# Kernel optimization log

Hardware: AMD Instinct MI355X
Metric: run time of the kernel (lower is better)

## Reference

```python
import jax, jax.numpy as jnp
import numpy as np

T, D, N, H = 2032, 1408, 16, 88  # K == N (MHA vision attention)
BLOCK_SIZE = 128
ROPE_THETA = 10000.0


def _apply_rope_interleaved(x_tnh, freqs_cis):
    # x_tnh: [T, N, H]; freqs_cis: [T, H//2, 2] with (..., 0)=cos, (..., 1)=sin.
    cos = freqs_cis[:, None, :, 0]  # [T, 1, H//2]
    sin = freqs_cis[:, None, :, 1]
    x1 = x_tnh[..., 0::2]
    x2 = x_tnh[..., 1::2]
    # interleaved rotation: pairs (even, odd) rotated by angle theta_t
    rot = jnp.stack([x1 * cos - x2 * sin, x1 * sin + x2 * cos], axis=-1)
    return rot.reshape(x_tnh.shape)


def setup_inputs() -> dict:
    key = jax.random.key(0)
    ks = jax.random.split(key, 10)
    s = 0.02
    x = jax.random.normal(ks[0], (T, D), dtype=jnp.float32)
    # precomputed rotary cos/sin table (interleaved ordering)
    pos = jnp.arange(T, dtype=jnp.float32)
    inv_freq = ROPE_THETA ** (-jnp.arange(0, H, 2, dtype=jnp.float32) / H)  # [H//2]
    ang = pos[:, None] * inv_freq[None, :]                                  # [T, H//2]
    freqs_cis = jnp.stack([jnp.cos(ang), jnp.sin(ang)], axis=-1)            # [T, H//2, 2]
    Wq = jax.random.normal(ks[1], (D, N, H), dtype=jnp.float32) * s
    Wk = jax.random.normal(ks[2], (D, N, H), dtype=jnp.float32) * s
    Wv = jax.random.normal(ks[3], (D, N, H), dtype=jnp.float32) * s
    Wo = jax.random.normal(ks[4], (N, H, D), dtype=jnp.float32) * s
    bq = jax.random.normal(ks[5], (N, H), dtype=jnp.float32) * s
    bk = jax.random.normal(ks[6], (N, H), dtype=jnp.float32) * s
    bv = jax.random.normal(ks[7], (N, H), dtype=jnp.float32) * s
    bo = jax.random.normal(ks[8], (D,), dtype=jnp.float32) * s
    return {"x": x, "freqs_cis": freqs_cis, "Wq": Wq, "bq": bq, "Wk": Wk,
            "bk": bk, "Wv": Wv, "bv": bv, "Wo": Wo, "bo": bo}


def reference(x, freqs_cis, Wq, bq, Wk, bk, Wv, bv, Wo, bo):
    t, d = x.shape
    n, h = bq.shape
    sm_scale = h ** -0.5
    # fused QKV projections + bias + RoPE (q, k only)
    q = jnp.einsum('td,dnh->tnh', x, Wq) + bq[None]
    q = _apply_rope_interleaved(q, freqs_cis)
    k = jnp.einsum('td,dkh->tkh', x, Wk) + bk[None]
    k = _apply_rope_interleaved(k, freqs_cis)
    v = jnp.einsum('td,dkh->tkh', x, Wv) + bv[None]
    # pad T up to a multiple of BLOCK_SIZE, as the flash-attention call requires
    pad_len = (BLOCK_SIZE - t % BLOCK_SIZE) % BLOCK_SIZE
    qp = jnp.pad(q, ((0, pad_len), (0, 0), (0, 0)))
    kp = jnp.pad(k, ((0, pad_len), (0, 0), (0, 0)))
    vp = jnp.pad(v, ((0, pad_len), (0, 0), (0, 0)))
    # [N, Tp, H]
    qh = jnp.transpose(qp, (1, 0, 2))
    kh = jnp.transpose(kp, (1, 0, 2))
    vh = jnp.transpose(vp, (1, 0, 2))
    # segment ids: 0 for valid tokens, 1 for padding; attention only within equal ids
    seg = jnp.concatenate([jnp.zeros((t,), jnp.int32), jnp.ones((pad_len,), jnp.int32)])
    mask = seg[:, None] == seg[None, :]  # [Tp, Tp]
    scores = jnp.einsum('nth,nsh->nts', qh, kh) * sm_scale
    scores = jnp.where(mask[None], scores, jnp.finfo(scores.dtype).min)
    probs = jax.nn.softmax(scores, axis=-1)
    out = jnp.einsum('nts,nsh->nth', probs, vh)        # [N, Tp, H]
    out = jnp.transpose(out, (1, 0, 2))[:t]            # [T, N, H]
    o = jnp.einsum('tnh,nhd->td', out, Wo) + bo
    return o
```

## Files before the change

kernel.cpp:

```cpp
#include <hip/hip_runtime.h>
#include <hip/hip_bf16.h>
#include <stdint.h>
#include <stddef.h>

typedef __bf16 bf16_t;
typedef __bf16 bf16x8 __attribute__((ext_vector_type(8)));
typedef __bf16 bf16x4 __attribute__((ext_vector_type(4)));
typedef float  f32x4  __attribute__((ext_vector_type(4)));

#define T_SEQ 2032
#define T_PAD 2048
#define DM    1408
#define NHEAD 16
#define HD    88
#define HP    96
#define KVB   128
#define NT    (T_PAD / KVB)
#define SM_SCALE 0.10660035817780521f
#define LOG2E 1.4426950408889634f
#define DEFER_THR 8.0f

__device__ __forceinline__ void gload_lds16(const bf16_t* g, bf16_t* l) {
  __builtin_amdgcn_global_load_lds(
      (__attribute__((address_space(1))) void*)(g),
      (__attribute__((address_space(3))) void*)(l), 16, 0, 0);
}

__global__ void k_convert_x(const float* __restrict__ x, bf16_t* __restrict__ Xb) {
  int idx = blockIdx.x * 256 + threadIdx.x;
  const int total = T_PAD * DM / 4;
  if (idx >= total) return;
  int base = idx * 4;
  int t = base / DM;
  float4 v;
  if (t < T_SEQ) v = *(const float4*)(x + base);
  else           v = make_float4(0.f, 0.f, 0.f, 0.f);
  bf16x4 o;
  o[0] = (bf16_t)v.x; o[1] = (bf16_t)v.y; o[2] = (bf16_t)v.z; o[3] = (bf16_t)v.w;
  *(bf16x4*)(Xb + base) = o;
}

__global__ void k_transpose4(const float* __restrict__ W0, const float* __restrict__ W1,
                             const float* __restrict__ W2, const float* __restrict__ W3,
                             bf16_t* __restrict__ d012, bf16_t* __restrict__ d3) {
  const int which = blockIdx.x / 484;
  const int b = blockIdx.x % 484;
  const float* src = (which == 0) ? W0 : (which == 1) ? W1 : (which == 2) ? W2 : W3;
  bf16_t* dst = (which < 3) ? (d012 + (size_t)which * DM * DM) : d3;
  const int tr = b / 22, tc = b % 22;
  __shared__ float tile[64][65];
  const int t = threadIdx.x;
  const int row = t >> 2, l4 = t & 3;
#pragma unroll
  for (int i = 0; i < 4; ++i) {
    float4 v = *(const float4*)(src + (size_t)(tr * 64 + row) * DM + tc * 64 + l4 * 16 + i * 4);
    *(float4*)&tile[row][l4 * 16 + i * 4] = v;
  }
  __syncthreads();
  const int jj = t >> 2;
#pragma unroll
  for (int it = 0; it < 2; ++it) {
    const int c = (t & 3) + 4 * it;
    bf16x8 o;
#pragma unroll
    for (int e = 0; e < 8; ++e) o[e] = (bf16_t)tile[c * 8 + e][jj];
    *(bf16x8*)(dst + (size_t)(tc * 64 + jj) * DM + tr * 64 + c * 8) = o;
  }
}

__device__ __forceinline__ void gemm_main_1408(
    const bf16_t* __restrict__ A, const bf16_t* __restrict__ Bt,
    bf16_t* As, bf16_t* Bs,
    int m0, int n0, f32x4 acc[4][4]) {
  const int tid = threadIdx.x;
  const int w = tid >> 6, lane = tid & 63;
  const int l15 = lane & 15, lg = lane >> 4;
  const int b0 = w * 2048 + lane * 16;
  const int r0 = b0 >> 6, k0 = (b0 & 63) >> 1;
  const int b1 = b0 + 1024;
  const int r1 = b1 >> 6, k1 = (b1 & 63) >> 1;
  const int wr = w >> 1, wc = w & 1;
  const size_t aoff0 = (size_t)(m0 + r0) * DM + k0;
  const size_t aoff1 = (size_t)(m0 + r1) * DM + k1;
  const size_t boff0 = (size_t)(n0 + r0) * DM + k0;
  const size_t boff1 = (size_t)(n0 + r1) * DM + k1;
  gload_lds16(A + aoff0, As + w * 1024);
  gload_lds16(A + aoff1, As + w * 1024 + 512);
  gload_lds16(Bt + boff0, Bs + w * 1024);
  gload_lds16(Bt + boff1, Bs + w * 1024 + 512);
  for (int kt = 0; kt < 44; ++kt) {
    const int cur = kt & 1;
    const int kon = ((kt < 43) ? kt + 1 : 43) * 32;
    const int db = (cur ^ 1) * 4096;
    gload_lds16(A + aoff0 + kon, As + db + w * 1024);
    gload_lds16(A + aoff1 + kon, As + db + w * 1024 + 512);
    gload_lds16(Bt + boff0 + kon, Bs + db + w * 1024);
    gload_lds16(Bt + boff1 + kon, Bs + db + w * 1024 + 512);
    asm volatile("s_waitcnt vmcnt(4)" ::: "memory");
    __builtin_amdgcn_s_barrier();
    const bf16_t* Ac = As + cur * 4096;
    const bf16_t* Bc = Bs + cur * 4096;
    bf16x8 av[4], bv[4];
#pragma unroll
    for (int m = 0; m < 4; ++m)
      av[m] = *(const bf16x8*)(Ac + (wr * 64 + m * 16 + l15) * 32 + lg * 8);
#pragma unroll
    for (int n = 0; n < 4; ++n)
      bv[n] = *(const bf16x8*)(Bc + (wc * 64 + n * 16 + l15) * 32 + lg * 8);
    __builtin_amdgcn_s_setprio(1);
#pragma unroll
    for (int m = 0; m < 4; ++m)
#pragma unroll
      for (int n = 0; n < 4; ++n)
        acc[m][n] = __builtin_amdgcn_mfma_f32_16x16x32_bf16(av[m], bv[n], acc[m][n], 0, 0, 0);
    __builtin_amdgcn_s_setprio(0);
    __builtin_amdgcn_s_barrier();
  }
  asm volatile("s_waitcnt vmcnt(0)" ::: "memory");
}

__global__ __launch_bounds__(256, 2) void k_gemm_qkv(
    const bf16_t* __restrict__ A, const bf16_t* __restrict__ Bt,
    const float* __restrict__ bq, const float* __restrict__ bk,
    const float* __restrict__ bvp, const float* __restrict__ freqs,
    bf16_t* __restrict__ Qh, bf16_t* __restrict__ Kh, bf16_t* __restrict__ Vt) {
  __shared__ bf16_t As[2 * 4096];
  __shared__ bf16_t Bs[2 * 4096];
  const int bid = blockIdx.x;
  const int sbid = (bid & 7) * 66 + (bid >> 3);
  const int mt = sbid / 33, nt = sbid % 33;
  f32x4 acc[4][4];
#pragma unroll
  for (int m = 0; m < 4; ++m)
#pragma unroll
    for (int n = 0; n < 4; ++n) acc[m][n] = (f32x4){0.f, 0.f, 0.f, 0.f};
  gemm_main_1408(A, Bt, As, Bs, mt * 128, nt * 128, acc);
  const int tid = threadIdx.x, w = tid >> 6, lane = tid & 63;
  const int l15 = lane & 15, lg = lane >> 4;
  const int wr = w >> 1, wc = w & 1;
  const int cb = nt * 128 + wc * 64, rb = mt * 128 + wr * 64;
#pragma unroll
  for (int n = 0; n < 4; ++n) {
    const int col = cb + n * 16 + l15;
    const int seg = (col >= 2 * DM) ? 2 : ((col >= DM) ? 1 : 0);
    const int cc = col - seg * DM;
    const float* bp = (seg == 0) ? bq : (seg == 1) ? bk : bvp;
    const float bval = bp[cc];
    const int hn = cc / 88;
    const int hh = cc - hn * 88;
    const int hbase = hh & ~1;
    const bool odd = hh & 1;
#pragma unroll
    for (int m = 0; m < 4; ++m) {
      const int tb = rb + m * 16 + lg * 4;
      if (seg == 2) {
        bf16x4 vv;
#pragma unroll
        for (int r = 0; r < 4; ++r) vv[r] = (bf16_t)(acc[m][n][r] + bval);
        *(bf16x4*)(Vt + ((size_t)hn * HP + hh) * T_PAD + tb) = vv;
      } else {
#pragma unroll
        for (int r = 0; r < 4; ++r) {
          const int t = tb + r;
          const float v = acc[m][n][r] + bval;
          const float p = __shfl_xor(v, 1);
          const int tc2 = (t < T_SEQ) ? t : 0;
          const float c = freqs[tc2 * 88 + hbase];
          const float s = freqs[tc2 * 88 + hbase + 1];
          const float x1 = odd ? p : v;
          const float x2 = odd ? v : p;
          const float ro = odd ? (x1 * s + x2 * c) : (x1 * c - x2 * s);
          if (seg == 0)
            Qh[((size_t)hn * T_PAD + t) * HP + hh] = (bf16_t)(ro * (SM_SCALE * LOG2E));
          else
            Kh[((size_t)hn * T_PAD + t) * HP + hh] = (bf16_t)ro;
        }
      }
    }
  }
}

__global__ __launch_bounds__(256, 2) void k_gemm_out64(
    const bf16_t* __restrict__ A, const bf16_t* __restrict__ Bt,
    const float* __restrict__ bo, float* __restrict__ out) {
  __shared__ bf16_t Sm[2 * 6144];
  const int bid = blockIdx.x;
  const int sbid = (bid & 7) * 44 + (bid >> 3);
  const int mt = sbid / 11, nt = sbid % 11;
  const int m0 = mt * 64, n0 = nt * 128;
  const int tid = threadIdx.x, w = tid >> 6, lane = tid & 63;
  const int l15 = lane & 15, lg = lane >> 4;
  const bf16_t* srcp[3];
  size_t srco[3];
  int dste[3];
#pragma unroll
  for (int p = 0; p < 3; ++p) {
    const int off = w * 3072 + p * 1024;
    const int o = off + lane * 16;
    dste[p] = off >> 1;
    if (off < 4096) {
      int r = o >> 6, k = (o & 63) >> 1;
      srcp[p] = A; srco[p] = (size_t)(m0 + r) * DM + k;
    } else {
      int ob = o - 4096;
      int r = ob >> 6, k = (ob & 63) >> 1;
      srcp[p] = Bt; srco[p] = (size_t)(n0 + r) * DM + k;
    }
  }
  f32x4 acc[4][2];
#pragma unroll
  for (int m = 0; m < 4; ++m)
#pragma unroll
    for (int n = 0; n < 2; ++n) acc[m][n] = (f32x4){0.f, 0.f, 0.f, 0.f};
#pragma unroll
  for (int p = 0; p < 3; ++p) gload_lds16(srcp[p] + srco[p], Sm + dste[p]);
  for (int kt = 0; kt < 44; ++kt) {
    const int cur = kt & 1;
    const int kon = ((kt < 43) ? kt + 1 : 43) * 32;
    const int db = (cur ^ 1) * 6144;
#pragma unroll
    for (int p = 0; p < 3; ++p)
      gload_lds16(srcp[p] + srco[p] + kon, Sm + db + dste[p]);
    asm volatile("s_waitcnt vmcnt(3)" ::: "memory");
    __builtin_amdgcn_s_barrier();
    const bf16_t* Sc = Sm + cur * 6144;
    bf16x8 av[4], bv2[2];
#pragma unroll
    for (int m = 0; m < 4; ++m)
      av[m] = *(const bf16x8*)(Sc + (m * 16 + l15) * 32 + lg * 8);
#pragma unroll
    for (int n = 0; n < 2; ++n)
      bv2[n] = *(const bf16x8*)(Sc + 2048 + (w * 32 + n * 16 + l15) * 32 + lg * 8);
    __builtin_amdgcn_s_setprio(1);
#pragma unroll
    for (int m = 0; m < 4; ++m)
#pragma unroll
      for (int n = 0; n < 2; ++n)
        acc[m][n] = __builtin_amdgcn_mfma_f32_16x16x32_bf16(av[m], bv2[n], acc[m][n], 0, 0, 0);
    __builtin_amdgcn_s_setprio(0);
    __builtin_amdgcn_s_barrier();
  }
  asm volatile("s_waitcnt vmcnt(0)" ::: "memory");
  const int cb = n0 + w * 32;
#pragma unroll
  for (int n = 0; n < 2; ++n) {
    const int col = cb + n * 16 + l15;
    const float bval = bo[col];
#pragma unroll
    for (int m = 0; m < 4; ++m) {
#pragma unroll
      for (int r = 0; r < 4; ++r) {
        const int t = m0 + m * 16 + lg * 4 + r;
        if (t < T_SEQ) out[(size_t)t * DM + col] = acc[m][n][r] + bval;
      }
    }
  }
}

__global__ __launch_bounds__(256, 2) void k_attn(
    const bf16_t* __restrict__ Qh, const bf16_t* __restrict__ Kh,
    const bf16_t* __restrict__ Vt, bf16_t* __restrict__ Ob) {
  __shared__ bf16_t Ps[4][16 * 136];
  const int tid = threadIdx.x;
  const int w = tid >> 6, lane = tid & 63;
  const int l15 = lane & 15, lg = lane >> 4;
  const int bid = blockIdx.x;
  const int sbid = (bid & 7) * 64 + (bid >> 3);
  const int head = sbid >> 5;
  const int qt = sbid & 31;
  const bf16_t* Qn = Qh + (size_t)head * T_PAD * HP;
  const bf16_t* Kn = Kh + (size_t)head * T_PAD * HP;
  const bf16_t* Vn = Vt + (size_t)head * HP * T_PAD;
  const int q0 = qt * 64 + w * 16;

  bf16x8 qf[3];
#pragma unroll
  for (int kh = 0; kh < 3; ++kh)
    qf[kh] = *(const bf16x8*)(Qn + (size_t)(q0 + l15) * HP + kh * 32 + lg * 8);

  f32x4 oacc[6];
#pragma unroll
  for (int j = 0; j < 6; ++j) oacc[j] = (f32x4){0.f, 0.f, 0.f, 0.f};
  float mrow = -1e30f;
  float lrowp = 0.f;

  for (int kvt = 0; kvt < NT; ++kvt) {
    const int s0 = kvt * KVB;
    f32x4 sf[8];
#pragma unroll
    for (int half = 0; half < 2; ++half) {
      bf16x8 kf[12];
#pragma unroll
      for (int ss = 0; ss < 4; ++ss)
#pragma unroll
        for (int kh = 0; kh < 3; ++kh)
          kf[ss * 3 + kh] = *(const bf16x8*)(
              Kn + (size_t)(s0 + (half * 4 + ss) * 16 + l15) * HP + kh * 32 + lg * 8);
      __builtin_amdgcn_s_setprio(1);
#pragma unroll
      for (int ss = 0; ss < 4; ++ss) {
        f32x4 s = {0.f, 0.f, 0.f, 0.f};
#pragma unroll
        for (int kh = 0; kh < 3; ++kh)
          s = __builtin_amdgcn_mfma_f32_16x16x32_bf16(kf[ss * 3 + kh], qf[kh], s, 0, 0, 0);
        sf[half * 4 + ss] = s;
      }
      __builtin_amdgcn_s_setprio(0);
    }
    bf16x8 vfA[12];
#pragma unroll
    for (int ks = 0; ks < 2; ++ks)
#pragma unroll
      for (int j = 0; j < 6; ++j)
        vfA[ks * 6 + j] = *(const bf16x8*)(
            Vn + (size_t)(j * 16 + l15) * T_PAD + s0 + ks * 32 + lg * 8);
    if (s0 + KVB > T_SEQ) {
#pragma unroll
      for (int ss = 0; ss < 8; ++ss)
#pragma unroll
        for (int r = 0; r < 4; ++r)
          if (s0 + ss * 16 + lg * 4 + r >= T_SEQ) sf[ss][r] = -1e30f;
    }
    float tm = sf[0][0];
#pragma unroll
    for (int ss = 0; ss < 8; ++ss)
#pragma unroll
      for (int r = 0; r < 4; ++r) tm = fmaxf(tm, sf[ss][r]);
    tm = fmaxf(tm, __shfl_xor(tm, 16));
    tm = fmaxf(tm, __shfl_xor(tm, 32));
    if (!__all(tm <= mrow + DEFER_THR)) {
      const float mn = fmaxf(mrow, tm);
      const float scv = __builtin_amdgcn_exp2f(mrow - mn);
      mrow = mn;
      lrowp *= scv;
#pragma unroll
      for (int r = 0; r < 4; ++r) {
        const float sq = __shfl(scv, lg * 4 + r, 16);
#pragma unroll
        for (int j = 0; j < 6; ++j) oacc[j][r] *= sq;
      }
    }
    float rs = 0.f;
#pragma unroll
    for (int ss = 0; ss < 8; ++ss)
#pragma unroll
      for (int r = 0; r < 4; ++r) {
        const float p = __builtin_amdgcn_exp2f(sf[ss][r] - mrow);
        rs += p;
        Ps[w][l15 * 136 + ss * 16 + lg * 4 + r] = (bf16_t)p;
      }
    lrowp += rs;
    bf16x8 vfB[12];
#pragma unroll
    for (int ks = 0; ks < 2; ++ks)
#pragma unroll
      for (int j = 0; j < 6; ++j)
        vfB[ks * 6 + j] = *(const bf16x8*)(
            Vn + (size_t)(j * 16 + l15) * T_PAD + s0 + (ks + 2) * 32 + lg * 8);
    __builtin_amdgcn_s_setprio(1);
#pragma unroll
    for (int ks = 0; ks < 2; ++ks) {
      bf16x8 pa = *(const bf16x8*)(&Ps[w][l15 * 136 + ks * 32 + lg * 8]);
#pragma unroll
      for (int j = 0; j < 6; ++j)
        oacc[j] = __builtin_amdgcn_mfma_f32_16x16x32_bf16(pa, vfA[ks * 6 + j], oacc[j], 0, 0, 0);
    }
#pragma unroll
    for (int ks = 0; ks < 2; ++ks) {
      bf16x8 pa = *(const bf16x8*)(&Ps[w][l15 * 136 + (ks + 2) * 32 + lg * 8]);
#pragma unroll
      for (int j = 0; j < 6; ++j)
        oacc[j] = __builtin_amdgcn_mfma_f32_16x16x32_bf16(pa, vfB[ks * 6 + j], oacc[j], 0, 0, 0);
    }
    __builtin_amdgcn_s_setprio(0);
  }
  lrowp += __shfl_xor(lrowp, 16);
  lrowp += __shfl_xor(lrowp, 32);
  float lq[4];
#pragma unroll
  for (int r = 0; r < 4; ++r) lq[r] = __shfl(lrowp, lg * 4 + r, 16);
#pragma unroll
  for (int j = 0; j < 6; ++j) {
    const int h = j * 16 + l15;
    if (h < HD) {
#pragma unroll
      for (int r = 0; r < 4; ++r) {
        const int t = q0 + lg * 4 + r;
        if (t < T_SEQ)
          Ob[(size_t)t * DM + head * HD + h] = (bf16_t)(oacc[j][r] / lq[r]);
      }
    }
  }
}

extern "C" void kernel_launch(void* const* d_in, const int* in_sizes, int n_in,
                              void* d_out, int out_size, void* d_ws, size_t ws_size,
                              hipStream_t stream) {
  (void)in_sizes; (void)n_in; (void)out_size;
  const float* x     = (const float*)d_in[0];
  const float* freqs = (const float*)d_in[1];
  const float* Wq    = (const float*)d_in[2];
  const float* bq    = (const float*)d_in[3];
  const float* Wk    = (const float*)d_in[4];
  const float* bk    = (const float*)d_in[5];
  const float* Wv    = (const float*)d_in[6];
  const float* bv    = (const float*)d_in[7];
  const float* Wo    = (const float*)d_in[8];
  const float* bo    = (const float*)d_in[9];
  float* out = (float*)d_out;
  char* ws = (char*)d_ws;

  bf16_t* Xb  = (bf16_t*)(ws);
  bf16_t* Wt  = (bf16_t*)(ws + 5767168);
  bf16_t* Qh  = (bf16_t*)(ws + 17661952);
  bf16_t* Kh  = (bf16_t*)(ws + 23953408);
  bf16_t* Vt  = (bf16_t*)(ws + 30244864);
  bf16_t* Ob  = Xb;
  const size_t NEED_ALL = 36536320ull + 3964928ull;
  const bool sep_wot = (ws_size >= NEED_ALL);
  bf16_t* Wot = sep_wot ? (bf16_t*)(ws + 36536320) : Wt;

  hipMemsetAsync(Qh, 0, 6291456, stream);

  k_convert_x<<<(T_PAD * DM / 4 + 255) / 256, 256, 0, stream>>>(x, Xb);
  if (sep_wot) {
    k_transpose4<<<4 * 484, 256, 0, stream>>>(Wq, Wk, Wv, Wo, Wt, Wot);
  } else {
    k_transpose4<<<3 * 484, 256, 0, stream>>>(Wq, Wk, Wv, Wo, Wt, Wot);
  }

  k_gemm_qkv<<<16 * 33, 256, 0, stream>>>(Xb, Wt, bq, bk, bv, freqs, Qh, Kh, Vt);

  if (!sep_wot)
    k_transpose4<<<484, 256, 0, stream>>>(Wo, Wo, Wo, Wo, Wot, Wot);

  k_attn<<<NHEAD * 32, 256, 0, stream>>>(Qh, Kh, Vt, Ob);
  k_gemm_out64<<<32 * 11, 256, 0, stream>>>(Ob, Wot, bo, out);
}
```

Baseline: 302.6 us.

## Stage K in swizzled double-buffered LDS, shrink KV and out-GEMM tiles

The attention kernel now prefetches 64-row K tiles into XOR-swizzled, double-buffered LDS using async global-to-LDS loads, instead of each wave reading K from global memory directly. The KV block shrinks from 128 to 64, and P is written as packed bf16 pairs. The V transpose stride is padded to 2112 to cut cache-set conflicts. The output GEMM switches to 64x64 tiles with twice as many blocks, and both GEMMs raise their launch-bound occupancy to 3; this adds per-tile barriers and gives up some reuse per block.

```diff
diff --git a/kernel.cpp b/kernel.cpp
--- a/kernel.cpp
+++ b/kernel.cpp
@@ -6,6 +6,7 @@
 typedef __bf16 bf16_t;
 typedef __bf16 bf16x8 __attribute__((ext_vector_type(8)));
 typedef __bf16 bf16x4 __attribute__((ext_vector_type(4)));
+typedef __bf16 bf16x2 __attribute__((ext_vector_type(2)));
 typedef float  f32x4  __attribute__((ext_vector_type(4)));
 
 #define T_SEQ 2032
@@ -14,7 +15,8 @@
 #define NHEAD 16
 #define HD    88
 #define HP    96
-#define KVB   128
+#define VST   2112
+#define KVB   64
 #define NT    (T_PAD / KVB)
 #define SM_SCALE 0.10660035817780521f
 #define LOG2E 1.4426950408889634f
@@ -70,8 +72,7 @@
 
 __device__ __forceinline__ void gemm_main_1408(
     const bf16_t* __restrict__ A, const bf16_t* __restrict__ Bt,
-    bf16_t* As, bf16_t* Bs,
-    int m0, int n0, f32x4 acc[4][4]) {
+    bf16_t* As, bf16_t* Bs, int m0, int n0, f32x4 acc[4][4]) {
   const int tid = threadIdx.x;
   const int w = tid >> 6, lane = tid & 63;
   const int l15 = lane & 15, lg = lane >> 4;
@@ -119,7 +120,7 @@
   asm volatile("s_waitcnt vmcnt(0)" ::: "memory");
 }
 
-__global__ __launch_bounds__(256, 2) void k_gemm_qkv(
+__global__ __launch_bounds__(256, 3) void k_gemm_qkv(
     const bf16_t* __restrict__ A, const bf16_t* __restrict__ Bt,
     const float* __restrict__ bq, const float* __restrict__ bk,
     const float* __restrict__ bvp, const float* __restrict__ freqs,
@@ -157,7 +158,7 @@
         bf16x4 vv;
 #pragma unroll
         for (int r = 0; r < 4; ++r) vv[r] = (bf16_t)(acc[m][n][r] + bval);
-        *(bf16x4*)(Vt + ((size_t)hn * HP + hh) * T_PAD + tb) = vv;
+        *(bf16x4*)(Vt + ((size_t)hn * HP + hh) * VST + tb) = vv;
       } else {
 #pragma unroll
         for (int r = 0; r < 4; ++r) {
@@ -180,22 +181,23 @@
   }
 }
 
-__global__ __launch_bounds__(256, 2) void k_gemm_out64(
+__global__ __launch_bounds__(256, 3) void k_gemm_out64(
     const bf16_t* __restrict__ A, const bf16_t* __restrict__ Bt,
     const float* __restrict__ bo, float* __restrict__ out) {
-  __shared__ bf16_t Sm[2 * 6144];
+  __shared__ bf16_t Sm[2 * 4096];
   const int bid = blockIdx.x;
-  const int sbid = (bid & 7) * 44 + (bid >> 3);
-  const int mt = sbid / 11, nt = sbid % 11;
-  const int m0 = mt * 64, n0 = nt * 128;
+  const int sbid = (bid & 7) * 88 + (bid >> 3);
+  const int mt = sbid / 22, nt = sbid % 22;
+  const int m0 = mt * 64, n0 = nt * 64;
   const int tid = threadIdx.x, w = tid >> 6, lane = tid & 63;
   const int l15 = lane & 15, lg = lane >> 4;
-  const bf16_t* srcp[3];
-  size_t srco[3];
-  int dste[3];
-#pragma unroll
-  for (int p = 0; p < 3; ++p) {
-    const int off = w * 3072 + p * 1024;
+  const int wr = w >> 1, wc = w & 1;
+  const bf16_t* srcp[2];
+  size_t srco[2];
+  int dste[2];
+#pragma unroll
+  for (int p = 0; p < 2; ++p) {
+    const int off = (w * 2 + p) * 1024;
     const int o = off + lane * 16;
     dste[p] = off >> 1;
     if (off < 4096) {
@@ -207,33 +209,33 @@
       srcp[p] = Bt; srco[p] = (size_t)(n0 + r) * DM + k;
     }
   }
-  f32x4 acc[4][2];
-#pragma unroll
-  for (int m = 0; m < 4; ++m)
+  f32x4 acc[2][2];
+#pragma unroll
+  for (int m = 0; m < 2; ++m)
 #pragma unroll
     for (int n = 0; n < 2; ++n) acc[m][n] = (f32x4){0.f, 0.f, 0.f, 0.f};
 #pragma unroll
-  for (int p = 0; p < 3; ++p) gload_lds16(srcp[p] + srco[p], Sm + dste[p]);
+  for (int p = 0; p < 2; ++p) gload_lds16(srcp[p] + srco[p], Sm + dste[p]);
   for (int kt = 0; kt < 44; ++kt) {
     const int cur = kt & 1;
     const int kon = ((kt < 43) ? kt + 1 : 43) * 32;
-    const int db = (cur ^ 1) * 6144;
-#pragma unroll
-    for (int p = 0; p < 3; ++p)
+    const int db = (cur ^ 1) * 4096;
+#pragma unroll
+    for (int p = 0; p < 2; ++p)
       gload_lds16(srcp[p] + srco[p] + kon, Sm + db + dste[p]);
-    asm volatile("s_waitcnt vmcnt(3)" ::: "memory");
-    __builtin_amdgcn_s_barrier();
-    const bf16_t* Sc = Sm + cur * 6144;
-    bf16x8 av[4], bv2[2];
-#pragma unroll
-    for (int m = 0; m < 4; ++m)
-      av[m] = *(const bf16x8*)(Sc + (m * 16 + l15) * 32 + lg * 8);
+    asm volatile("s_waitcnt vmcnt(2)" ::: "memory");
+    __builtin_amdgcn_s_barrier();
+    const bf16_t* Sc = Sm + cur * 4096;
+    bf16x8 av[2], bv2[2];
+#pragma unroll
+    for (int m = 0; m < 2; ++m)
+      av[m] = *(const bf16x8*)(Sc + (wr * 32 + m * 16 + l15) * 32 + lg * 8);
 #pragma unroll
     for (int n = 0; n < 2; ++n)
-      bv2[n] = *(const bf16x8*)(Sc + 2048 + (w * 32 + n * 16 + l15) * 32 + lg * 8);
+      bv2[n] = *(const bf16x8*)(Sc + 2048 + (wc * 32 + n * 16 + l15) * 32 + lg * 8);
     __builtin_amdgcn_s_setprio(1);
 #pragma unroll
-    for (int m = 0; m < 4; ++m)
+    for (int m = 0; m < 2; ++m)
 #pragma unroll
       for (int n = 0; n < 2; ++n)
         acc[m][n] = __builtin_amdgcn_mfma_f32_16x16x32_bf16(av[m], bv2[n], acc[m][n], 0, 0, 0);
@@ -241,16 +243,15 @@
     __builtin_amdgcn_s_barrier();
   }
   asm volatile("s_waitcnt vmcnt(0)" ::: "memory");
-  const int cb = n0 + w * 32;
 #pragma unroll
   for (int n = 0; n < 2; ++n) {
-    const int col = cb + n * 16 + l15;
+    const int col = n0 + wc * 32 + n * 16 + l15;
     const float bval = bo[col];
 #pragma unroll
-    for (int m = 0; m < 4; ++m) {
+    for (int m = 0; m < 2; ++m) {
 #pragma unroll
       for (int r = 0; r < 4; ++r) {
-        const int t = m0 + m * 16 + lg * 4 + r;
+        const int t = m0 + wr * 32 + m * 16 + lg * 4 + r;
         if (t < T_SEQ) out[(size_t)t * DM + col] = acc[m][n][r] + bval;
       }
     }
@@ -260,17 +261,19 @@
 __global__ __launch_bounds__(256, 2) void k_attn(
     const bf16_t* __restrict__ Qh, const bf16_t* __restrict__ Kh,
     const bf16_t* __restrict__ Vt, bf16_t* __restrict__ Ob) {
-  __shared__ bf16_t Ps[4][16 * 136];
+  __shared__ bf16_t Ks[2][KVB * 128];
+  __shared__ bf16_t Ps[4][16 * 72];
   const int tid = threadIdx.x;
   const int w = tid >> 6, lane = tid & 63;
   const int l15 = lane & 15, lg = lane >> 4;
+  const int swz = l15 & 7;
   const int bid = blockIdx.x;
   const int sbid = (bid & 7) * 64 + (bid >> 3);
   const int head = sbid >> 5;
   const int qt = sbid & 31;
   const bf16_t* Qn = Qh + (size_t)head * T_PAD * HP;
   const bf16_t* Kn = Kh + (size_t)head * T_PAD * HP;
-  const bf16_t* Vn = Vt + (size_t)head * HP * T_PAD;
+  const bf16_t* Vn = Vt + (size_t)head * HP * VST;
   const int q0 = qt * 64 + w * 16;
 
   bf16x8 qf[3];
@@ -284,46 +287,59 @@
   float mrow = -1e30f;
   float lrowp = 0.f;
 
+  int kro[4], kco[4];
+#pragma unroll
+  for (int p = 0; p < 4; ++p) {
+    int o = (w * 4 + p) * 1024 + lane * 16;
+    int row = o >> 8, ch = (o >> 4) & 15;
+    kro[p] = row; kco[p] = (ch ^ (row & 7)) << 3;
+  }
+#pragma unroll
+  for (int p = 0; p < 4; ++p)
+    gload_lds16(Kn + (size_t)kro[p] * HP + kco[p], &Ks[0][(w * 4 + p) * 512]);
+
   for (int kvt = 0; kvt < NT; ++kvt) {
     const int s0 = kvt * KVB;
-    f32x4 sf[8];
-#pragma unroll
-    for (int half = 0; half < 2; ++half) {
-      bf16x8 kf[12];
+    const int cur = kvt & 1;
+    const int nxt = (kvt < NT - 1) ? kvt + 1 : kvt;
+#pragma unroll
+    for (int p = 0; p < 4; ++p)
+      gload_lds16(Kn + (size_t)(nxt * KVB + kro[p]) * HP + kco[p],
+                  &Ks[cur ^ 1][(w * 4 + p) * 512]);
+    asm volatile("s_waitcnt vmcnt(4)" ::: "memory");
+    __builtin_amdgcn_s_barrier();
+
+    const bf16_t* Kc = Ks[cur];
+    f32x4 sf[4];
+    __builtin_amdgcn_s_setprio(1);
+#pragma unroll
+    for (int ss = 0; ss < 4; ++ss) {
+      f32x4 s = {0.f, 0.f, 0.f, 0.f};
+#pragma unroll
+      for (int kh = 0; kh < 3; ++kh) {
+        bf16x8 kf = *(const bf16x8*)(Kc + (ss * 16 + l15) * 128 + (((kh * 4 + lg) ^ swz) << 3));
+        s = __builtin_amdgcn_mfma_f32_16x16x32_bf16(kf, qf[kh], s, 0, 0, 0);
+      }
+      sf[ss] = s;
+    }
+    __builtin_amdgcn_s_setprio(0);
+    bf16x8 vf[12];
+#pragma unroll
+    for (int ks = 0; ks < 2; ++ks)
+#pragma unroll
+      for (int j = 0; j < 6; ++j)
+        vf[ks * 6 + j] = *(const bf16x8*)(
+            Vn + (size_t)(j * 16 + l15) * VST + s0 + ks * 32 + lg * 8);
+    if (s0 + KVB > T_SEQ) {
 #pragma unroll
       for (int ss = 0; ss < 4; ++ss)
-#pragma unroll
-        for (int kh = 0; kh < 3; ++kh)
-          kf[ss * 3 + kh] = *(const bf16x8*)(
-              Kn + (size_t)(s0 + (half * 4 + ss) * 16 + l15) * HP + kh * 32 + lg * 8);
-      __builtin_amdgcn_s_setprio(1);
-#pragma unroll
-      for (int ss = 0; ss < 4; ++ss) {
-        f32x4 s = {0.f, 0.f, 0.f, 0.f};
-#pragma unroll
-        for (int kh = 0; kh < 3; ++kh)
-          s = __builtin_amdgcn_mfma_f32_16x16x32_bf16(kf[ss * 3 + kh], qf[kh], s, 0, 0, 0);
-        sf[half * 4 + ss] = s;
-      }
-      __builtin_amdgcn_s_setprio(0);
-    }
-    bf16x8 vfA[12];
-#pragma unroll
-    for (int ks = 0; ks < 2; ++ks)
-#pragma unroll
-      for (int j = 0; j < 6; ++j)
-        vfA[ks * 6 + j] = *(const bf16x8*)(
-            Vn + (size_t)(j * 16 + l15) * T_PAD + s0 + ks * 32 + lg * 8);
-    if (s0 + KVB > T_SEQ) {
-#pragma unroll
-      for (int ss = 0; ss < 8; ++ss)
 #pragma unroll
         for (int r = 0; r < 4; ++r)
           if (s0 + ss * 16 + lg * 4 + r >= T_SEQ) sf[ss][r] = -1e30f;
     }
     float tm = sf[0][0];
 #pragma unroll
-    for (int ss = 0; ss < 8; ++ss)
+    for (int ss = 0; ss < 4; ++ss)
 #pragma unroll
       for (int r = 0; r < 4; ++r) tm = fmaxf(tm, sf[ss][r]);
     tm = fmaxf(tm, __shfl_xor(tm, 16));
@@ -342,38 +358,29 @@
     }
     float rs = 0.f;
 #pragma unroll
-    for (int ss = 0; ss < 8; ++ss)
-#pragma unroll
-      for (int r = 0; r < 4; ++r) {
-        const float p = __builtin_amdgcn_exp2f(sf[ss][r] - mrow);
-        rs += p;
-        Ps[w][l15 * 136 + ss * 16 + lg * 4 + r] = (bf16_t)p;
+    for (int ss = 0; ss < 4; ++ss)
+#pragma unroll
+      for (int jj = 0; jj < 2; ++jj) {
+        const float p0 = __builtin_amdgcn_exp2f(sf[ss][2 * jj] - mrow);
+        const float p1 = __builtin_amdgcn_exp2f(sf[ss][2 * jj + 1] - mrow);
+        rs += p0 + p1;
+        bf16x2 pk; pk[0] = (bf16_t)p0; pk[1] = (bf16_t)p1;
+        *(bf16x2*)(&Ps[w][l15 * 72 + ss * 16 + lg * 4 + 2 * jj]) = pk;
       }
     lrowp += rs;
-    bf16x8 vfB[12];
-#pragma unroll
-    for (int ks = 0; ks < 2; ++ks)
+    __builtin_amdgcn_s_setprio(1);
+#pragma unroll
+    for (int ks = 0; ks < 2; ++ks) {
+      bf16x8 pa = *(const bf16x8*)(&Ps[w][l15 * 72 + ks * 32 + lg * 8]);
 #pragma unroll
       for (int j = 0; j < 6; ++j)
-        vfB[ks * 6 + j] = *(const bf16x8*)(
-            Vn + (size_t)(j * 16 + l15) * T_PAD + s0 + (ks + 2) * 32 + lg * 8);
-    __builtin_amdgcn_s_setprio(1);
-#pragma unroll
-    for (int ks = 0; ks < 2; ++ks) {
-      bf16x8 pa = *(const bf16x8*)(&Ps[w][l15 * 136 + ks * 32 + lg * 8]);
-#pragma unroll
-      for (int j = 0; j < 6; ++j)
-        oacc[j] = __builtin_amdgcn_mfma_f32_16x16x32_bf16(pa, vfA[ks * 6 + j], oacc[j], 0, 0, 0);
-    }
-#pragma unroll
-    for (int ks = 0; ks < 2; ++ks) {
-      bf16x8 pa = *(const bf16x8*)(&Ps[w][l15 * 136 + (ks + 2) * 32 + lg * 8]);
-#pragma unroll
-      for (int j = 0; j < 6; ++j)
-        oacc[j] = __builtin_amdgcn_mfma_f32_16x16x32_bf16(pa, vfB[ks * 6 + j], oacc[j], 0, 0, 0);
+        oacc[j] = __builtin_amdgcn_mfma_f32_16x16x32_bf16(pa, vf[ks * 6 + j], oacc[j], 0, 0, 0);
     }
     __builtin_amdgcn_s_setprio(0);
-  }
+    __builtin_amdgcn_s_barrier();
+  }
+  asm volatile("s_waitcnt vmcnt(0)" ::: "memory");
+
   lrowp += __shfl_xor(lrowp, 16);
   lrowp += __shfl_xor(lrowp, 32);
   float lq[4];
@@ -416,9 +423,9 @@
   bf16_t* Kh  = (bf16_t*)(ws + 23953408);
   bf16_t* Vt  = (bf16_t*)(ws + 30244864);
   bf16_t* Ob  = Xb;
-  const size_t NEED_ALL = 36536320ull + 3964928ull;
+  const size_t NEED_ALL = 36732928ull + 3964928ull;
   const bool sep_wot = (ws_size >= NEED_ALL);
-  bf16_t* Wot = sep_wot ? (bf16_t*)(ws + 36536320) : Wt;
+  bf16_t* Wot = sep_wot ? (bf16_t*)(ws + 36732928) : Wt;
 
   hipMemsetAsync(Qh, 0, 6291456, stream);
 
@@ -435,5 +442,5 @@
     k_transpose4<<<484, 256, 0, stream>>>(Wo, Wo, Wo, Wo, Wot, Wot);
 
   k_attn<<<NHEAD * 32, 256, 0, stream>>>(Qh, Kh, Vt, Ob);
-  k_gemm_out64<<<32 * 11, 256, 0, stream>>>(Ob, Wot, bo, out);
-}
+  k_gemm_out64<<<32 * 22, 256, 0, stream>>>(Ob, Wot, bo, out);
+}
```

Measured after the change: 277.9 us. 8.2% less time.
